# Optimization experiments

Measured on AMD Instinct MI355X. Metric: run time of the kernel, lower is better.

The kernel has to match this reference:

```python
import math
import jax, jax.numpy as jnp
import numpy as np

B, T, D = 8, 2048, 512
EPS = 1e-5


def _gate(x, W, b, a, g, beta):
    # Linear -> PReLU (single shared slope a) -> LayerNorm -> sigmoid
    h = x @ W.T + b
    h = jnp.where(h >= 0, h, a * h)
    mu = jnp.mean(h, axis=-1, keepdims=True)
    var = jnp.var(h, axis=-1, keepdims=True)
    h = (h - mu) / jnp.sqrt(var + EPS) * g + beta
    return jax.nn.sigmoid(h)


def setup_inputs() -> dict:
    key = jax.random.key(0)
    ks = jax.random.split(key, 12)
    lin = lambda k: jax.random.normal(k, (D, D), jnp.float32) * 0.02
    z = jnp.zeros((D,), jnp.float32)
    o = jnp.ones((D,), jnp.float32)
    a0 = jnp.float32(0.25)  # PReLU default init
    inp = {
        "query": jax.random.normal(ks[0], (B, T, D), jnp.float32),
        "value": jax.random.normal(ks[1], (B, T, D), jnp.float32),
        "aux_emb": jax.random.normal(ks[2], (B, 1, D), jnp.float32),
        # ragged valid lengths in [T//2, T] to keep every sample realistic
        "input_len": jax.random.randint(ks[3], (B,), T // 2, T + 1),
        "Wq": lin(ks[4]), "bq": z,
        "Wqg": lin(ks[5]), "bqg": z, "aq": a0, "gq": o, "betaq": z,
        "Wkg": lin(ks[6]), "bkg": z, "ak": a0, "gk": o, "betak": z,
        "Wvg": lin(ks[7]), "bvg": z, "av": a0, "gv": o, "betav": z,
        "Wsig": lin(ks[8]), "bsig": z,
        "Wtan": lin(ks[9]), "btan": z,
    }
    return inp


def reference(query, value, aux_emb, input_len,
              Wq, bq,
              Wqg, bqg, aq, gq, betaq,
              Wkg, bkg, ak, gk, betak,
              Wvg, bvg, av, gv, betav,
              Wsig, bsig, Wtan, btan):
    q = query @ Wq.T + bq
    q = q * _gate(aux_emb, Wqg, bqg, aq, gq, betaq)          # [B,T,D]
    k = value * _gate(aux_emb, Wkg, bkg, ak, gk, betak)      # [B,T,D]
    vg = _gate(aux_emb, Wvg, bvg, av, gv, betav)             # [B,1,D]
    vg = jax.nn.sigmoid(vg @ Wsig.T + bsig) * jnp.tanh(vg @ Wtan.T + btan)
    v = value * vg                                           # [B,T,D]

    w = jnp.einsum('btd,bsd->bts', q, k) / math.sqrt(D)      # [B,T,T]
    r = jnp.arange(T)
    causal = (r[:, None] >= r[None, :]).astype(w.dtype)      # tril ones
    w = w * causal
    w = jnp.where(w == 0.0, -jnp.inf, w)  # torch quirk: exact zeros -> -inf
    L = input_len[:, None, None]                              # [B,1,1]
    invalid = (r[None, :, None] < L) & (r[None, None, :] >= L)
    w = jnp.where(invalid, -jnp.inf, w)
    p = jax.nn.softmax(w, axis=-1)
    # rows beyond input_len are padding: zero them (torch code produced NaN
    # there via -inf*0; intended semantics is zeroed padding rows)
    row_valid = (r[None, :, None] < L).astype(p.dtype)        # [B,T,1]
    p = p * row_valid
    return p @ v                                              # [B,T,D]
```

## Files before the change

kernel.cpp:

```cpp
#include <hip/hip_runtime.h>
#include <hip/hip_bf16.h>
#include <stdint.h>

#define BB 8
#define TT 2048
#define DD 512

typedef __attribute__((ext_vector_type(8))) __bf16 bf16x8;
typedef __attribute__((ext_vector_type(4))) float f32x4;

__device__ __forceinline__ unsigned short f2bf(float f) {
    unsigned u = __builtin_bit_cast(unsigned, f);
    unsigned r = u + 0x7fffu + ((u >> 16) & 1u);
    return (unsigned short)(r >> 16);
}

__device__ __forceinline__ void gload_lds16(const unsigned short* g, unsigned short* l) {
    __builtin_amdgcn_global_load_lds(
        (const __attribute__((address_space(1))) void*)g,
        (__attribute__((address_space(3))) void*)l, 16, 0, 0);
}

__global__ __launch_bounds__(256) void gates_mv1(
    const float* __restrict__ aux,
    const float* __restrict__ Wqg, const float* __restrict__ bqg, const float* __restrict__ aq,
    const float* __restrict__ Wkg, const float* __restrict__ bkg, const float* __restrict__ ak,
    const float* __restrict__ Wvg, const float* __restrict__ bvg, const float* __restrict__ av,
    float* __restrict__ h) {
    __shared__ float saux[BB * DD];
    int tid = threadIdx.x;
#pragma unroll
    for (int i = 0; i < 4; i++) {
        int idx = tid + i * 256;
        ((float4*)saux)[idx] = ((const float4*)aux)[idx];
    }
    __syncthreads();
    int wave = (blockIdx.x * 256 + tid) >> 6;
    int lane = tid & 63;
    int g = wave >> 9, r = wave & 511;
    const float* W    = (g == 0) ? Wqg : (g == 1) ? Wkg : Wvg;
    const float* bias = (g == 0) ? bqg : (g == 1) ? bkg : bvg;
    const float* alpha = (g == 0) ? aq : (g == 1) ? ak : av;
    const float4* Wrow = (const float4*)(W + (size_t)r * DD);
    float acc[BB];
#pragma unroll
    for (int b = 0; b < BB; b++) acc[b] = 0.f;
#pragma unroll
    for (int c = 0; c < 2; c++) {
        float4 w4 = Wrow[lane + c * 64];
#pragma unroll
        for (int b = 0; b < BB; b++) {
            float4 a4 = ((const float4*)(saux + b * DD))[lane + c * 64];
            acc[b] += w4.x * a4.x + w4.y * a4.y + w4.z * a4.z + w4.w * a4.w;
        }
    }
#pragma unroll
    for (int b = 0; b < BB; b++) {
#pragma unroll
        for (int s = 1; s < 64; s <<= 1) acc[b] += __shfl_xor(acc[b], s, 64);
    }
    if (lane == 0) {
        float bi = bias[r], a = alpha[0];
#pragma unroll
        for (int b = 0; b < BB; b++) {
            float v = acc[b] + bi;
            v = (v >= 0.f) ? v : a * v;
            h[(g * BB + b) * DD + r] = v;
        }
    }
}

__global__ __launch_bounds__(512) void gates_norm(
    const float* __restrict__ h,
    const float* __restrict__ gq, const float* __restrict__ betaq,
    const float* __restrict__ gk, const float* __restrict__ betak,
    const float* __restrict__ gv, const float* __restrict__ betav,
    float* __restrict__ qgate, float* __restrict__ kgate, float* __restrict__ vg) {
    int g = blockIdx.x >> 3, b = blockIdx.x & 7, tid = threadIdx.x;
    __shared__ float red[DD], red2[DD];
    float hv = h[(g * BB + b) * DD + tid];
    red[tid] = hv; red2[tid] = hv * hv;
    __syncthreads();
    for (int s = 256; s > 0; s >>= 1) {
        if (tid < s) { red[tid] += red[tid + s]; red2[tid] += red2[tid + s]; }
        __syncthreads();
    }
    float mu = red[0] * (1.f / DD);
    float var = red2[0] * (1.f / DD) - mu * mu;
    const float* gg = (g == 0) ? gq : (g == 1) ? gk : gv;
    const float* be = (g == 0) ? betaq : (g == 1) ? betak : betav;
    float val = (hv - mu) * rsqrtf(var + 1e-5f) * gg[tid] + be[tid];
    float sg = 1.f / (1.f + expf(-val));
    float* outp = (g == 0) ? qgate : (g == 1) ? kgate : vg;
    outp[b * DD + tid] = sg;
}

__global__ __launch_bounds__(256) void gates_mv2(
    const float* __restrict__ vg,
    const float* __restrict__ Wsig, const float* __restrict__ bsig,
    const float* __restrict__ Wtan, const float* __restrict__ btan,
    float* __restrict__ vgate) {
    __shared__ float svg[BB * DD];
    int tid = threadIdx.x;
#pragma unroll
    for (int i = 0; i < 4; i++) {
        int idx = tid + i * 256;
        ((float4*)svg)[idx] = ((const float4*)vg)[idx];
    }
    __syncthreads();
    int r = (blockIdx.x * 256 + tid) >> 6;
    int lane = tid & 63;
    const float4* Ws = (const float4*)(Wsig + (size_t)r * DD);
    const float4* Wt = (const float4*)(Wtan + (size_t)r * DD);
    float as_[BB], at_[BB];
#pragma unroll
    for (int b = 0; b < BB; b++) { as_[b] = 0.f; at_[b] = 0.f; }
#pragma unroll
    for (int c = 0; c < 2; c++) {
        float4 w1 = Ws[lane + c * 64];
        float4 w2 = Wt[lane + c * 64];
#pragma unroll
        for (int b = 0; b < BB; b++) {
            float4 a4 = ((const float4*)(svg + b * DD))[lane + c * 64];
            as_[b] += w1.x * a4.x + w1.y * a4.y + w1.z * a4.z + w1.w * a4.w;
            at_[b] += w2.x * a4.x + w2.y * a4.y + w2.z * a4.z + w2.w * a4.w;
        }
    }
#pragma unroll
    for (int b = 0; b < BB; b++) {
#pragma unroll
        for (int s = 1; s < 64; s <<= 1) {
            as_[b] += __shfl_xor(as_[b], s, 64);
            at_[b] += __shfl_xor(at_[b], s, 64);
        }
    }
    if (lane == 0) {
        float b1 = bsig[r], b2 = btan[r];
#pragma unroll
        for (int b = 0; b < BB; b++) {
            float s1 = 1.f / (1.f + expf(-(as_[b] + b1)));
            float s2 = tanhf(at_[b] + b2);
            vgate[b * DD + r] = s1 * s2;
        }
    }
}

__global__ __launch_bounds__(256) void convert_kernel(
    const float* __restrict__ query, const float* __restrict__ Wq,
    const float* __restrict__ value,
    const float* __restrict__ kgate, const float* __restrict__ vgate,
    unsigned short* __restrict__ queryb, unsigned short* __restrict__ Wqb,
    unsigned short* __restrict__ kb, unsigned short* __restrict__ vbT) {
    __shared__ float tile[32][33];
    int bi = blockIdx.x, tid = threadIdx.x;
    if (bi < 8192) {
        int idx = bi * 256 + tid;
        float4 q4 = ((const float4*)query)[idx];
        ushort4 oq;
        oq.x = f2bf(q4.x); oq.y = f2bf(q4.y); oq.z = f2bf(q4.z); oq.w = f2bf(q4.w);
        ((ushort4*)queryb)[idx] = oq;
    } else if (bi < 8448) {
        int idx = (bi - 8192) * 256 + tid;
        float4 w4 = ((const float4*)Wq)[idx];
        ushort4 o;
        o.x = f2bf(w4.x); o.y = f2bf(w4.y); o.z = f2bf(w4.z); o.w = f2bf(w4.w);
        ((ushort4*)Wqb)[idx] = o;
    } else {
        int vb = bi - 8448;
        int tIdx = vb & 63, dIdx = (vb >> 6) & 15, b = vb >> 10;
        int t0 = tIdx * 32, d0 = dIdx * 32;
        int tx = tid & 31, ty = tid >> 5;
        float kg = kgate[b * DD + d0 + tx];
#pragma unroll
        for (int i = 0; i < 4; i++) {
            int t = t0 + ty + i * 8;
            float v = value[((size_t)b * TT + t) * DD + d0 + tx];
            tile[ty + i * 8][tx] = v;
            kb[((size_t)b * TT + t) * DD + d0 + tx] = f2bf(v * kg);
        }
        __syncthreads();
#pragma unroll
        for (int i = 0; i < 4; i++) {
            int d = d0 + ty + i * 8;
            float g = vgate[b * DD + d];
            vbT[((size_t)b * DD + d) * TT + t0 + tx] = f2bf(tile[tx][ty + i * 8] * g);
        }
    }
}

#define STAGE_AB(BUF, K0)                                                                 \
    _Pragma("unroll") for (int i = 0; i < 2; i++) {                                       \
        int idx = tid * 8 + i * 2048;                                                     \
        int r = idx >> 5;                                                                 \
        int cg = ((idx >> 3) & 3) ^ ((r >> 1) & 3);                                       \
        gload_lds16(&Ap_[(size_t)r * lda_ + (K0) + cg * 8], &As[BUF][idx]);               \
        gload_lds16(&Bp_[(size_t)r * ldb_ + (K0) + cg * 8], &Bs[BUF][idx]);               \
    }

#define GEMM_CORE(APTR, ALDA, BPTR, BLDA, KSTART, KEND)                                   \
    __shared__ __align__(16) unsigned short As[2][128 * 32];                              \
    __shared__ __align__(16) unsigned short Bs[2][128 * 32];                              \
    const unsigned short* Ap_ = (APTR);                                                   \
    const unsigned short* Bp_ = (BPTR);                                                   \
    const int lda_ = (ALDA), ldb_ = (BLDA);                                               \
    int tid = threadIdx.x;                                                                \
    int lane = tid & 63, wid = tid >> 6;                                                  \
    int wm = (wid >> 1) * 64, wn = (wid & 1) * 64;                                        \
    int lm = lane & 15, quad = lane >> 4;                                                 \
    f32x4 acc[4][4];                                                                      \
    _Pragma("unroll") for (int im = 0; im < 4; im++)                                      \
        _Pragma("unroll") for (int in = 0; in < 4; in++)                                  \
            acc[im][in] = (f32x4){0.f, 0.f, 0.f, 0.f};                                    \
    STAGE_AB(0, (KSTART))                                                                 \
    int cur_ = 0;                                                                         \
    for (int k0 = (KSTART); k0 < (KEND); k0 += 32) {                                      \
        __syncthreads();                                                                  \
        if (k0 + 32 < (KEND)) { STAGE_AB(cur_ ^ 1, k0 + 32) }                             \
        bf16x8 af[4], bf_[4];                                                             \
        _Pragma("unroll") for (int i = 0; i < 4; i++) {                                   \
            int row = wm + i * 16 + lm;                                                   \
            af[i] = *(const bf16x8*)&As[cur_][row * 32 + (quad ^ ((row >> 1) & 3)) * 8];  \
        }                                                                                 \
        _Pragma("unroll") for (int i = 0; i < 4; i++) {                                   \
            int row = wn + i * 16 + lm;                                                   \
            bf_[i] = *(const bf16x8*)&Bs[cur_][row * 32 + (quad ^ ((row >> 1) & 3)) * 8]; \
        }                                                                                 \
        _Pragma("unroll") for (int im = 0; im < 4; im++)                                  \
            _Pragma("unroll") for (int in = 0; in < 4; in++)                              \
                acc[im][in] = __builtin_amdgcn_mfma_f32_16x16x32_bf16(af[im], bf_[in],    \
                                                                     acc[im][in], 0, 0, 0);\
        cur_ ^= 1;                                                                        \
    }

__global__ __launch_bounds__(256) void qgemm_kernel(
    const unsigned short* __restrict__ Amat, const unsigned short* __restrict__ Bmat,
    const float* __restrict__ bq, const float* __restrict__ qgate,
    unsigned short* __restrict__ qb) {
    int m0 = blockIdx.x * 128, n0 = blockIdx.y * 128;
    const unsigned short* Ap = Amat + (size_t)m0 * DD;
    const unsigned short* Bp = Bmat + (size_t)n0 * DD;
    GEMM_CORE(Ap, DD, Bp, DD, 0, DD)
    int b = m0 >> 11;
#pragma unroll
    for (int im = 0; im < 4; im++) {
        int row = m0 + wm + im * 16 + quad * 4;
#pragma unroll
        for (int in = 0; in < 4; in++) {
            int col = n0 + wn + in * 16 + lm;
            float bias = bq[col];
            float g = qgate[b * DD + col];
#pragma unroll
            for (int r = 0; r < 4; r++) {
                float v = (acc[im][in][r] + bias) * g;
                qb[(size_t)(row + r) * DD + col] = f2bf(v);
            }
        }
    }
}

__global__ __launch_bounds__(512) void attn_kernel(
    const unsigned short* __restrict__ qb, const unsigned short* __restrict__ kb,
    const unsigned short* __restrict__ vbT, const int* __restrict__ input_len,
    float* __restrict__ out) {
    int bid = blockIdx.x;
    int p = bid >> 3, b = bid & 7;
    int L = input_len[b];
    int tid = threadIdx.x;
    int lane = tid & 63, w = tid >> 6;
    int lm = lane & 15, quad = lane >> 4;
    const size_t bTT = (size_t)b * TT;
    const float scale = 0.044194173824159216f;

    __shared__ __align__(16) unsigned short Qs[32 * 512];
    __shared__ __align__(16) unsigned short KV[2][2048 * 8];
    __shared__ __align__(16) unsigned short Ps[32 * 256];
    __shared__ float rs_lds[32];

#define STAGE_K(DST, KV0, D0)                                                     \
    _Pragma("unroll") for (int i_ = 0; i_ < 4; i_++) {                            \
        int idx_ = tid + i_ * 512;                                                \
        int r_ = idx_ >> 3, c_ = idx_ & 7;                                        \
        int g_ = c_ ^ (r_ & 7);                                                   \
        gload_lds16(&kb[(bTT + (KV0) + r_) * DD + (D0) + g_ * 8],                 \
                    &KV[DST][idx_ * 8]);                                          \
    }
#define STAGE_V(DST, KVC)                                                         \
    _Pragma("unroll") for (int i_ = 0; i_ < 4; i_++) {                            \
        int idx_ = tid + i_ * 512;                                                \
        int r_ = idx_ >> 2, c_ = idx_ & 3;                                        \
        int g_ = c_ ^ (r_ & 3);                                                   \
        gload_lds16(&vbT[((size_t)(b * DD) + r_) * TT + (KVC) + g_ * 8],          \
                    &KV[DST][idx_ * 8]);                                          \
    }

#pragma unroll 1
    for (int half = 0; half < 2; half++) {
        int strip = half ? (63 - p) : p;
        int t0 = strip * 32;
        int nk = (strip >> 3) + 1;

        __syncthreads();
#pragma unroll
        for (int i_ = 0; i_ < 4; i_++) {
            int idx_ = tid + i_ * 512;
            int r_ = idx_ >> 6, c_ = idx_ & 63;
            int gc_ = (c_ & 56) | ((c_ ^ r_) & 7);
            gload_lds16(&qb[(bTT + t0 + r_) * DD + gc_ * 8], &Qs[idx_ * 8]);
        }
        STAGE_K(0, 0, 0)
        int buf = 0;

        f32x4 oacc[2][4];
#pragma unroll
        for (int mi = 0; mi < 2; mi++)
#pragma unroll
            for (int ni = 0; ni < 4; ni++) oacc[mi][ni] = (f32x4){0.f, 0.f, 0.f, 0.f};
        float rsum[2][4];
#pragma unroll
        for (int mi = 0; mi < 2; mi++)
#pragma unroll
            for (int r = 0; r < 4; r++) rsum[mi][r] = 0.f;

        for (int m = 0; m < nk; m++) {
            int kv0 = m * 256;
            f32x4 sacc[2][2];
#pragma unroll
            for (int mi = 0; mi < 2; mi++)
#pragma unroll
                for (int ni = 0; ni < 2; ni++) sacc[mi][ni] = (f32x4){0.f, 0.f, 0.f, 0.f};

#pragma unroll 1
            for (int ds = 0; ds < 8; ds++) {
                __syncthreads();
                if (ds < 7) { STAGE_K(buf ^ 1, kv0, (ds + 1) * 64) }
                else        { STAGE_V(buf ^ 1, kv0) }
#pragma unroll
                for (int kk = 0; kk < 2; kk++) {
                    bf16x8 aq[2], bk[2];
#pragma unroll
                    for (int mi = 0; mi < 2; mi++) {
                        int row = mi * 16 + lm;
                        int c = ds * 8 + kk * 4 + quad;
                        int sc = (c & 56) | ((c ^ row) & 7);
                        aq[mi] = *(const bf16x8*)&Qs[(row << 9) + sc * 8];
                    }
#pragma unroll
                    for (int ni = 0; ni < 2; ni++) {
                        int row = w * 32 + ni * 16 + lm;
                        int sc = (kk * 4 + quad) ^ (row & 7);
                        bk[ni] = *(const bf16x8*)&KV[buf][(row << 6) + sc * 8];
                    }
#pragma unroll
                    for (int mi = 0; mi < 2; mi++)
#pragma unroll
                        for (int ni = 0; ni < 2; ni++)
                            sacc[mi][ni] = __builtin_amdgcn_mfma_f32_16x16x32_bf16(
                                aq[mi], bk[ni], sacc[mi][ni], 0, 0, 0);
                }
                buf ^= 1;
            }

#pragma unroll
            for (int mi = 0; mi < 2; mi++)
#pragma unroll
                for (int ni = 0; ni < 2; ni++)
#pragma unroll
                    for (int r = 0; r < 4; r++) {
                        int trow = mi * 16 + quad * 4 + r;
                        int t = t0 + trow;
                        int e = w * 32 + ni * 16 + lm;
                        int s = kv0 + e;
                        float pv = (s <= t) ? expf(sacc[mi][ni][r] * scale) : 0.f;
                        rsum[mi][r] += pv;
                        int c = e >> 3, o = e & 7;
                        int sc = (c & 24) | ((c ^ trow) & 7);
                        Ps[trow * 256 + sc * 8 + o] = f2bf(pv);
                    }

#pragma unroll 1
            for (int kc = 0; kc < 8; kc++) {
                __syncthreads();
                if (kc < 7)           { STAGE_V(buf ^ 1, kv0 + (kc + 1) * 32) }
                else if (m + 1 < nk)  { STAGE_K(buf ^ 1, kv0 + 256, 0) }
                bf16x8 pa[2], vb[4];
#pragma unroll
                for (int mi = 0; mi < 2; mi++) {
                    int row = mi * 16 + lm;
                    int c = kc * 4 + quad;
                    int sc = (c & 24) | ((c ^ row) & 7);
                    pa[mi] = *(const bf16x8*)&Ps[row * 256 + sc * 8];
                }
#pragma unroll
                for (int ni = 0; ni < 4; ni++) {
                    int row = w * 64 + ni * 16 + lm;
                    int sc = quad ^ (row & 3);
                    vb[ni] = *(const bf16x8*)&KV[buf][(row << 5) + sc * 8];
                }
#pragma unroll
                for (int mi = 0; mi < 2; mi++)
#pragma unroll
                    for (int ni = 0; ni < 4; ni++)
                        oacc[mi][ni] = __builtin_amdgcn_mfma_f32_16x16x32_bf16(
                            pa[mi], vb[ni], oacc[mi][ni], 0, 0, 0);
                buf ^= 1;
            }
        }

        __syncthreads();
        if (tid < 32) rs_lds[tid] = 0.f;
        __syncthreads();
#pragma unroll
        for (int mi = 0; mi < 2; mi++)
#pragma unroll
            for (int r = 0; r < 4; r++) {
                float v = rsum[mi][r];
                v += __shfl_xor(v, 1, 64);
                v += __shfl_xor(v, 2, 64);
                v += __shfl_xor(v, 4, 64);
                v += __shfl_xor(v, 8, 64);
                if (lm == 0) atomicAdd(&rs_lds[mi * 16 + quad * 4 + r], v);
            }
        __syncthreads();
#pragma unroll
        for (int mi = 0; mi < 2; mi++)
#pragma unroll
            for (int r = 0; r < 4; r++) {
                int trow = mi * 16 + quad * 4 + r;
                int t = t0 + trow;
                float inv = 1.f / rs_lds[trow];
                bool valid = (t < L);
#pragma unroll
                for (int ni = 0; ni < 4; ni++) {
                    int n = w * 64 + ni * 16 + lm;
                    float o = valid ? oacc[mi][ni][r] * inv : 0.f;
                    out[(bTT + t) * DD + n] = o;
                }
            }
    }
#undef STAGE_K
#undef STAGE_V
}

extern "C" void kernel_launch(void* const* d_in, const int* in_sizes, int n_in,
                              void* d_out, int out_size, void* d_ws, size_t ws_size,
                              hipStream_t stream) {
    const float* query = (const float*)d_in[0];
    const float* value = (const float*)d_in[1];
    const float* aux   = (const float*)d_in[2];
    const int*   ilen  = (const int*)d_in[3];
    const float* Wq    = (const float*)d_in[4];
    const float* bq    = (const float*)d_in[5];
    const float* Wqg   = (const float*)d_in[6];
    const float* bqg   = (const float*)d_in[7];
    const float* aq    = (const float*)d_in[8];
    const float* gq    = (const float*)d_in[9];
    const float* betaq = (const float*)d_in[10];
    const float* Wkg   = (const float*)d_in[11];
    const float* bkg   = (const float*)d_in[12];
    const float* ak    = (const float*)d_in[13];
    const float* gk    = (const float*)d_in[14];
    const float* betak = (const float*)d_in[15];
    const float* Wvg   = (const float*)d_in[16];
    const float* bvg   = (const float*)d_in[17];
    const float* av    = (const float*)d_in[18];
    const float* gv    = (const float*)d_in[19];
    const float* betav = (const float*)d_in[20];
    const float* Wsig  = (const float*)d_in[21];
    const float* bsig  = (const float*)d_in[22];
    const float* Wtan  = (const float*)d_in[23];
    const float* btan  = (const float*)d_in[24];

    char* ws = (char*)d_ws;
    float* qgate          = (float*)(ws + 0);
    float* kgate          = (float*)(ws + 16384);
    float* vgate          = (float*)(ws + 32768);
    unsigned short* Wqb   = (unsigned short*)(ws + 114688);
    unsigned short* queryb= (unsigned short*)(ws + 638976);
    unsigned short* qb    = (unsigned short*)(ws + 17416192);
    unsigned short* kb    = (unsigned short*)(ws + 34193408);
    unsigned short* vbT   = (unsigned short*)(ws + 50970624);
    float* hbuf           = (float*)(ws + 67747840);
    float* vg             = (float*)(ws + 67747840 + 49152);

    gates_mv1<<<384, 256, 0, stream>>>(aux, Wqg, bqg, aq, Wkg, bkg, ak, Wvg, bvg, av, hbuf);
    gates_norm<<<24, 512, 0, stream>>>(hbuf, gq, betaq, gk, betak, gv, betav,
                                       qgate, kgate, vg);
    gates_mv2<<<128, 256, 0, stream>>>(vg, Wsig, bsig, Wtan, btan, vgate);

    convert_kernel<<<16640, 256, 0, stream>>>(query, Wq, value, kgate, vgate,
                                              queryb, Wqb, kb, vbT);
    qgemm_kernel<<<dim3((BB * TT) / 128, DD / 128), 256, 0, stream>>>(queryb, Wqb, bq, qgate, qb);
    attn_kernel<<<256, 512, 0, stream>>>(qb, kb, vbT, ilen, (float*)d_out);
}
```

Before: 302.9 us.

## Load K and V fragments directly from global memory instead of LDS staging

Drops the double-buffered LDS staging of K and V tiles. Each wave now reads its private K rows and V^T rows straight from global memory into MFMA operand registers, with the inner loops fully unrolled. This removes the per-step block barriers and the LDS traffic for K/V, and frees 64KB of LDS, which may allow more blocks per CU. In exchange it gives up the async prefetch overlap and depends on cache hits and global latency hiding, with strided 16-byte accesses per lane.

```diff
diff --git a/kernel.cpp b/kernel.cpp
--- a/kernel.cpp
+++ b/kernel.cpp
@@ -272,26 +272,11 @@
     const float scale = 0.044194173824159216f;
 
     __shared__ __align__(16) unsigned short Qs[32 * 512];
-    __shared__ __align__(16) unsigned short KV[2][2048 * 8];
     __shared__ __align__(16) unsigned short Ps[32 * 256];
     __shared__ float rs_lds[32];
 
-#define STAGE_K(DST, KV0, D0)                                                     \
-    _Pragma("unroll") for (int i_ = 0; i_ < 4; i_++) {                            \
-        int idx_ = tid + i_ * 512;                                                \
-        int r_ = idx_ >> 3, c_ = idx_ & 7;                                        \
-        int g_ = c_ ^ (r_ & 7);                                                   \
-        gload_lds16(&kb[(bTT + (KV0) + r_) * DD + (D0) + g_ * 8],                 \
-                    &KV[DST][idx_ * 8]);                                          \
-    }
-#define STAGE_V(DST, KVC)                                                         \
-    _Pragma("unroll") for (int i_ = 0; i_ < 4; i_++) {                            \
-        int idx_ = tid + i_ * 512;                                                \
-        int r_ = idx_ >> 2, c_ = idx_ & 3;                                        \
-        int g_ = c_ ^ (r_ & 3);                                                   \
-        gload_lds16(&vbT[((size_t)(b * DD) + r_) * TT + (KVC) + g_ * 8],          \
-                    &KV[DST][idx_ * 8]);                                          \
-    }
+    const unsigned short* kw = kb + (bTT + (size_t)w * 32) * DD;
+    const unsigned short* vw = vbT + ((size_t)b * DD + (size_t)w * 64) * TT;
 
 #pragma unroll 1
     for (int half = 0; half < 2; half++) {
@@ -307,8 +292,8 @@
             int gc_ = (c_ & 56) | ((c_ ^ r_) & 7);
             gload_lds16(&qb[(bTT + t0 + r_) * DD + gc_ * 8], &Qs[idx_ * 8]);
         }
-        STAGE_K(0, 0, 0)
-        int buf = 0;
+        if (tid < 32) rs_lds[tid] = 0.f;
+        __syncthreads();
 
         f32x4 oacc[2][4];
 #pragma unroll
@@ -321,22 +306,25 @@
 #pragma unroll
             for (int r = 0; r < 4; r++) rsum[mi][r] = 0.f;
 
+#pragma unroll 1
         for (int m = 0; m < nk; m++) {
             int kv0 = m * 256;
+            const unsigned short* kwm = kw + (size_t)kv0 * DD;
             f32x4 sacc[2][2];
 #pragma unroll
             for (int mi = 0; mi < 2; mi++)
 #pragma unroll
                 for (int ni = 0; ni < 2; ni++) sacc[mi][ni] = (f32x4){0.f, 0.f, 0.f, 0.f};
 
-#pragma unroll 1
+#pragma unroll
             for (int ds = 0; ds < 8; ds++) {
-                __syncthreads();
-                if (ds < 7) { STAGE_K(buf ^ 1, kv0, (ds + 1) * 64) }
-                else        { STAGE_V(buf ^ 1, kv0) }
 #pragma unroll
                 for (int kk = 0; kk < 2; kk++) {
                     bf16x8 aq[2], bk[2];
+#pragma unroll
+                    for (int ni = 0; ni < 2; ni++)
+                        bk[ni] = *(const bf16x8*)&kwm[(size_t)(ni * 16 + lm) * DD +
+                                                      ds * 64 + (kk * 4 + quad) * 8];
 #pragma unroll
                     for (int mi = 0; mi < 2; mi++) {
                         int row = mi * 16 + lm;
@@ -345,21 +333,15 @@
                         aq[mi] = *(const bf16x8*)&Qs[(row << 9) + sc * 8];
                     }
 #pragma unroll
-                    for (int ni = 0; ni < 2; ni++) {
-                        int row = w * 32 + ni * 16 + lm;
-                        int sc = (kk * 4 + quad) ^ (row & 7);
-                        bk[ni] = *(const bf16x8*)&KV[buf][(row << 6) + sc * 8];
-                    }
-#pragma unroll
                     for (int mi = 0; mi < 2; mi++)
 #pragma unroll
                         for (int ni = 0; ni < 2; ni++)
                             sacc[mi][ni] = __builtin_amdgcn_mfma_f32_16x16x32_bf16(
                                 aq[mi], bk[ni], sacc[mi][ni], 0, 0, 0);
                 }
-                buf ^= 1;
             }
 
+            __syncthreads();
 #pragma unroll
             for (int mi = 0; mi < 2; mi++)
 #pragma unroll
@@ -376,13 +358,15 @@
                         int sc = (c & 24) | ((c ^ trow) & 7);
                         Ps[trow * 256 + sc * 8 + o] = f2bf(pv);
                     }
-
-#pragma unroll 1
+            __syncthreads();
+
+#pragma unroll
             for (int kc = 0; kc < 8; kc++) {
-                __syncthreads();
-                if (kc < 7)           { STAGE_V(buf ^ 1, kv0 + (kc + 1) * 32) }
-                else if (m + 1 < nk)  { STAGE_K(buf ^ 1, kv0 + 256, 0) }
-                bf16x8 pa[2], vb[4];
+                bf16x8 pa[2], vv[4];
+#pragma unroll
+                for (int ni = 0; ni < 4; ni++)
+                    vv[ni] = *(const bf16x8*)&vw[(size_t)(ni * 16 + lm) * TT +
+                                                 kv0 + kc * 32 + quad * 8];
 #pragma unroll
                 for (int mi = 0; mi < 2; mi++) {
                     int row = mi * 16 + lm;
@@ -391,23 +375,14 @@
                     pa[mi] = *(const bf16x8*)&Ps[row * 256 + sc * 8];
                 }
 #pragma unroll
-                for (int ni = 0; ni < 4; ni++) {
-                    int row = w * 64 + ni * 16 + lm;
-                    int sc = quad ^ (row & 3);
-                    vb[ni] = *(const bf16x8*)&KV[buf][(row << 5) + sc * 8];
-                }
-#pragma unroll
                 for (int mi = 0; mi < 2; mi++)
 #pragma unroll
                     for (int ni = 0; ni < 4; ni++)
                         oacc[mi][ni] = __builtin_amdgcn_mfma_f32_16x16x32_bf16(
-                            pa[mi], vb[ni], oacc[mi][ni], 0, 0, 0);
-                buf ^= 1;
+                            pa[mi], vv[ni], oacc[mi][ni], 0, 0, 0);
             }
         }
 
-        __syncthreads();
-        if (tid < 32) rs_lds[tid] = 0.f;
         __syncthreads();
 #pragma unroll
         for (int mi = 0; mi < 2; mi++)
@@ -437,8 +412,6 @@
                 }
             }
     }
-#undef STAGE_K
-#undef STAGE_V
 }
 
 extern "C" void kernel_launch(void* const* d_in, const int* in_sizes, int n_in,
```

New measurement: 331.0 us. 9.3% more time.
